# Optimization experiments

Measured on AMD Instinct MI355X. Metric: run time of the kernel, lower is better.

Reference implementation:

```python
import jax, jax.numpy as jnp
import numpy as np

N, D, B, K, H, E = 100000, 128, 4096, 64, 256, 128
DIN = D + 1
DELAYED_REWARD_STEP = 100.0


def setup_inputs() -> dict:
    key = jax.random.key(0)
    ks = jax.random.split(key, 16)
    s = 0.02
    d = {}
    d["node_pre_embedding"] = jax.random.normal(ks[0], (N, D), jnp.float32)
    d["steps"] = jax.random.uniform(ks[1], (B,), jnp.float32) * 50.0
    d["h0"] = jax.random.normal(ks[2], (B, H), jnp.float32) * 0.1
    d["c0"] = jax.random.normal(ks[3], (B, H), jnp.float32) * 0.1
    # MLP1: D_in -> 256 -> 128 (action embed, feeds LSTM input)
    d["W1a"] = jax.random.normal(ks[4], (256, DIN), jnp.float32) * s
    d["b1a"] = jnp.zeros((256,), jnp.float32)
    d["W1b"] = jax.random.normal(ks[5], (128, 256), jnp.float32) * s
    d["b1b"] = jnp.zeros((128,), jnp.float32)
    # MLP2: D_in -> 256 -> 128 (neighbor graph embed)
    d["W2a"] = jax.random.normal(ks[6], (256, DIN), jnp.float32) * s
    d["b2a"] = jnp.zeros((256,), jnp.float32)
    d["W2b"] = jax.random.normal(ks[7], (128, 256), jnp.float32) * s
    d["b2b"] = jnp.zeros((128,), jnp.float32)
    # MLP3: lstm_hidden (256) -> 128, single linear (hidden_dims3=[128])
    d["W3"] = jax.random.normal(ks[8], (E, H), jnp.float32) * s
    d["b3"] = jnp.zeros((E,), jnp.float32)
    # LSTMCell (PyTorch layout: gates i,f,g,o stacked on dim 0)
    d["Wih"] = jax.random.normal(ks[9], (4 * H, 128), jnp.float32) * s
    d["Whh"] = jax.random.normal(ks[10], (4 * H, H), jnp.float32) * s
    d["bih"] = jnp.zeros((4 * H,), jnp.float32)
    d["bhh"] = jnp.zeros((4 * H,), jnp.float32)
    # packed ragged adjacency: padded neighbor ids + per-row degree
    d["actions0"] = jax.random.randint(ks[11], (B,), 0, N)
    d["neighbors"] = jax.random.randint(ks[12], (B, K), 0, N)
    d["deg"] = jax.random.randint(ks[13], (B,), 1, K + 1)
    return d


def reference(node_pre_embedding, steps, h0, c0,
              W1a, b1a, W1b, b1b, W2a, b2a, W2b, b2b, W3, b3,
              Wih, Whh, bih, bhh, actions0, neighbors, deg):
    step_scaled = steps / DELAYED_REWARD_STEP  # [B]

    # --- graph embeddings for padded neighbors (ragged gather + MLP2) ---
    nei_feat = node_pre_embedding[neighbors]  # [B, K, D]
    step_col = jnp.broadcast_to(step_scaled[:, None, None], (B, K, 1))
    pre = jnp.concatenate([nei_feat, step_col], axis=-1)  # [B, K, D_in]
    g = jax.nn.relu(jnp.einsum('bkd,hd->bkh', pre, W2a) + b2a)
    g = jnp.einsum('bkh,eh->bke', g, W2b) + b2b  # [B, K, E]

    # --- action embedding: MLP1 -> LSTMCell -> MLP3 ---
    a_pre = jnp.concatenate([node_pre_embedding[actions0], step_scaled[:, None]], axis=-1)
    x = jax.nn.relu(a_pre @ W1a.T + b1a) @ W1b.T + b1b  # [B, 128]
    gates = x @ Wih.T + bih + h0 @ Whh.T + bhh  # [B, 4H]
    i, f, gg, o = jnp.split(gates, 4, axis=-1)
    c = jax.nn.sigmoid(f) * c0 + jax.nn.sigmoid(i) * jnp.tanh(gg)
    h = jax.nn.sigmoid(o) * jnp.tanh(c)
    emb = h @ W3.T + b3  # [B, E]

    # --- scaled dot-product scores, masked at padding ---
    vals = jnp.einsum('bke,be->bk', g, emb) / jnp.sqrt(jnp.float32(E))
    mask = jnp.arange(K)[None, :] < jnp.maximum(deg, 1)[:, None]
    vals = jnp.where(mask, vals, 0.0)
    return vals, h, c
```

## Files before the change

### kernel.cpp

```cpp
#include <hip/hip_runtime.h>
#include <hip/hip_bf16.h>

#define NN 100000
#define DD 128
#define BB 4096
#define KK 64
#define HH 256
#define EE 128

typedef __bf16 bf16x8 __attribute__((ext_vector_type(8)));
typedef float f32x4 __attribute__((ext_vector_type(4)));

#define EL_W1A 0
#define EL_W1B 32768
#define EL_WIH 65536
#define EL_WHH 196608
#define EL_W3  458752
#define EL_W2B 491520
#define EL_W2A 524288

#define BOFF_GB     0x110000
#define BOFF_W1COL  0x111000
#define BOFF_W2COL  0x111400
#define BOFF_CONST  0x111800
#define BOFF_X1     0x115800
#define BOFF_X      0x315800
#define BOFF_H0B    0x415800
#define BOFF_HB     0x615800
#define BOFF_EMB    0x815800
#define BOFF_T      0x915800

__device__ __forceinline__ float sigmoid_f(float x){ return 1.0f/(1.0f+__expf(-x)); }
__device__ __forceinline__ float tanh_f(float x){ return 1.0f - 2.0f/(__expf(2.0f*x)+1.0f); }

__device__ __forceinline__ bf16x8 pack8(float4 a, float4 b){
    bf16x8 v;
    v[0]=(__bf16)a.x; v[1]=(__bf16)a.y; v[2]=(__bf16)a.z; v[3]=(__bf16)a.w;
    v[4]=(__bf16)b.x; v[5]=(__bf16)b.y; v[6]=(__bf16)b.z; v[7]=(__bf16)b.w;
    return v;
}

__global__ __launch_bounds__(64) void swz_kernel(
    const float* __restrict__ W1a, const float* __restrict__ W1b,
    const float* __restrict__ Wih, const float* __restrict__ Whh,
    const float* __restrict__ W3,  const float* __restrict__ W2b,
    const float* __restrict__ W2a, const float* __restrict__ bih,
    const float* __restrict__ bhh, const float* __restrict__ h0,
    __bf16* __restrict__ wsbf, float* __restrict__ gb_ws,
    float* __restrict__ w1col_ws, float* __restrict__ w2col_ws,
    __bf16* __restrict__ h0_bf)
{
    int g = blockIdx.x, lane = threadIdx.x;
    if (g >= 1088){
        if (g < 1104){ int idx = (g-1088)*64 + lane; gb_ws[idx] = bih[idx] + bhh[idx]; }
        else if (g < 1108){ int idx = (g-1104)*64 + lane; w1col_ws[idx] = W1a[idx*129 + 128]; }
        else if (g < 1112){ int idx = (g-1108)*64 + lane; w2col_ws[idx] = W2a[idx*129 + 128]; }
        else {
            long i = (long)(g-1112)*64 + lane;
            const float4* sp = (const float4*)h0 + i*2;
            ((bf16x8*)h0_bf)[i] = pack8(sp[0], sp[1]);
        }
        return;
    }
    int quad = lane >> 4, l15 = lane & 15;
    const float* src; int stride, nkk, local; long dst; bool kn = false;
    if      (g <  64){ src=W1a; stride=129; nkk=4; dst=EL_W1A; local=g;      }
    else if (g < 128){ src=W1b; stride=256; nkk=8; dst=EL_W1B; local=g-64;   }
    else if (g < 384){ src=Wih; stride=128; nkk=4; dst=EL_WIH; local=g-128;  }
    else if (g < 896){ src=Whh; stride=256; nkk=8; dst=EL_WHH; local=g-384;  }
    else if (g < 960){ src=W3;  stride=256; nkk=8; dst=EL_W3;  local=g-896;  }
    else if (g <1024){ src=W2b; stride=256; nkk=4; dst=EL_W2B; local=g-960; kn=true; }
    else             { src=W2a; stride=129; nkk=4; dst=EL_W2A; local=g-1024; }
    int nt = local / nkk, kk = local % nkk;
    int n = nt*16 + l15, k0 = kk*32 + quad*8;
    bf16x8 v;
#pragma unroll
    for (int j = 0; j < 8; ++j){
        float x = kn ? src[(long)(k0+j)*stride + n] : src[(long)n*stride + k0 + j];
        v[j] = (__bf16)x;
    }
    ((bf16x8*)(wsbf + dst))[local*64 + lane] = v;
}

__global__ __launch_bounds__(64) void s1_kernel(
    const float* __restrict__ node_pre, const float* __restrict__ steps,
    const int* __restrict__ actions0, const float* __restrict__ b1a,
    const float* __restrict__ w1col, const __bf16* __restrict__ wsbf,
    __bf16* __restrict__ x1_bf)
{
    int lane = threadIdx.x, quad = lane >> 4, l15 = lane & 15;
    int mt = blockIdx.x >> 2, ng = blockIdx.x & 3, m0 = mt*16;
    long arow = actions0[m0 + l15];
    bf16x8 af[4];
#pragma unroll
    for (int kk = 0; kk < 4; ++kk){
        const float4* p = (const float4*)(node_pre + arow*128 + kk*32 + quad*8);
        af[kk] = pack8(p[0], p[1]);
    }
    float sb_i[4];
#pragma unroll
    for (int i = 0; i < 4; ++i) sb_i[i] = steps[m0 + quad*4 + i] * 0.01f;
    const bf16x8* FB = (const bf16x8*)(wsbf + EL_W1A);
#pragma unroll
    for (int j = 0; j < 4; ++j){
        int nt = ng*4 + j;
        f32x4 acc = {0.f,0.f,0.f,0.f};
#pragma unroll
        for (int kk = 0; kk < 4; ++kk)
            acc = __builtin_amdgcn_mfma_f32_16x16x32_bf16(af[kk], FB[(nt*4+kk)*64 + lane], acc, 0,0,0);
        int col = nt*16 + l15;
        float bb = b1a[col], wc = w1col[col];
#pragma unroll
        for (int i = 0; i < 4; ++i)
            x1_bf[(long)(m0 + quad*4 + i)*256 + col] = (__bf16)fmaxf(acc[i] + bb + wc*sb_i[i], 0.f);
    }
}

__global__ __launch_bounds__(64) void s2_kernel(
    const __bf16* __restrict__ x1_bf, const float* __restrict__ b1b,
    const __bf16* __restrict__ wsbf, __bf16* __restrict__ x_bf)
{
    int lane = threadIdx.x, quad = lane >> 4, l15 = lane & 15;
    int mt = blockIdx.x >> 2, ng = blockIdx.x & 3, m0 = mt*16;
    bf16x8 af[8];
#pragma unroll
    for (int kk = 0; kk < 8; ++kk)
        af[kk] = *(const bf16x8*)&x1_bf[(long)(m0 + l15)*256 + kk*32 + quad*8];
    const bf16x8* FB = (const bf16x8*)(wsbf + EL_W1B);
#pragma unroll
    for (int j = 0; j < 2; ++j){
        int nt = ng*2 + j;
        f32x4 acc = {0.f,0.f,0.f,0.f};
#pragma unroll
        for (int kk = 0; kk < 8; ++kk)
            acc = __builtin_amdgcn_mfma_f32_16x16x32_bf16(af[kk], FB[(nt*8+kk)*64 + lane], acc, 0,0,0);
        int col = nt*16 + l15;
        float bb = b1b[col];
#pragma unroll
        for (int i = 0; i < 4; ++i)
            x_bf[(long)(m0 + quad*4 + i)*128 + col] = (__bf16)(acc[i] + bb);
    }
}

__global__ __launch_bounds__(64) void lstm_kernel(
    const __bf16* __restrict__ x_bf, const __bf16* __restrict__ h0_bf,
    const float* __restrict__ c0_in, const float* __restrict__ gb_ws,
    const __bf16* __restrict__ wsbf,
    float* __restrict__ out_h, float* __restrict__ out_c, __bf16* __restrict__ h_bf)
{
    int lane = threadIdx.x, quad = lane >> 4, l15 = lane & 15;
    int mt = blockIdx.x >> 4, ct = blockIdx.x & 15, m0 = mt*16;
    bf16x8 af[12];
#pragma unroll
    for (int kk = 0; kk < 4; ++kk)
        af[kk] = *(const bf16x8*)&x_bf[(long)(m0 + l15)*128 + kk*32 + quad*8];
#pragma unroll
    for (int kk = 0; kk < 8; ++kk)
        af[4+kk] = *(const bf16x8*)&h0_bf[(long)(m0 + l15)*256 + kk*32 + quad*8];

    const bf16x8* FIH = (const bf16x8*)(wsbf + EL_WIH);
    const bf16x8* FHH = (const bf16x8*)(wsbf + EL_WHH);
    f32x4 aI = {0.f,0.f,0.f,0.f}, aF = aI, aG = aI, aO = aI;
#pragma unroll
    for (int kk = 0; kk < 4; ++kk){
        aI = __builtin_amdgcn_mfma_f32_16x16x32_bf16(af[kk], FIH[(( 0+ct)*4+kk)*64 + lane], aI, 0,0,0);
        aF = __builtin_amdgcn_mfma_f32_16x16x32_bf16(af[kk], FIH[((16+ct)*4+kk)*64 + lane], aF, 0,0,0);
        aG = __builtin_amdgcn_mfma_f32_16x16x32_bf16(af[kk], FIH[((32+ct)*4+kk)*64 + lane], aG, 0,0,0);
        aO = __builtin_amdgcn_mfma_f32_16x16x32_bf16(af[kk], FIH[((48+ct)*4+kk)*64 + lane], aO, 0,0,0);
    }
#pragma unroll
    for (int k2 = 0; k2 < 8; ++k2){
        aI = __builtin_amdgcn_mfma_f32_16x16x32_bf16(af[4+k2], FHH[(( 0+ct)*8+k2)*64 + lane], aI, 0,0,0);
        aF = __builtin_amdgcn_mfma_f32_16x16x32_bf16(af[4+k2], FHH[((16+ct)*8+k2)*64 + lane], aF, 0,0,0);
        aG = __builtin_amdgcn_mfma_f32_16x16x32_bf16(af[4+k2], FHH[((32+ct)*8+k2)*64 + lane], aG, 0,0,0);
        aO = __builtin_amdgcn_mfma_f32_16x16x32_bf16(af[4+k2], FHH[((48+ct)*8+k2)*64 + lane], aO, 0,0,0);
    }
    int col = ct*16 + l15;
    float bI = gb_ws[col], bF = gb_ws[256+col], bG = gb_ws[512+col], bO = gb_ws[768+col];
#pragma unroll
    for (int i = 0; i < 4; ++i){
        long row = m0 + quad*4 + i;
        float iv = aI[i]+bI, fv = aF[i]+bF, gv = aG[i]+bG, ov = aO[i]+bO;
        float cc = c0_in[row*256 + col];
        float cn = sigmoid_f(fv)*cc + sigmoid_f(iv)*tanh_f(gv);
        float hn = sigmoid_f(ov)*tanh_f(cn);
        out_c[row*256 + col] = cn;
        out_h[row*256 + col] = hn;
        h_bf[row*256 + col] = (__bf16)hn;
    }
}

__global__ __launch_bounds__(64) void s4_kernel(
    const __bf16* __restrict__ h_bf, const float* __restrict__ b3,
    const __bf16* __restrict__ wsbf, __bf16* __restrict__ emb_bf)
{
    int lane = threadIdx.x, quad = lane >> 4, l15 = lane & 15;
    int mt = blockIdx.x >> 2, ng = blockIdx.x & 3, m0 = mt*16;
    bf16x8 af[8];
#pragma unroll
    for (int kk = 0; kk < 8; ++kk)
        af[kk] = *(const bf16x8*)&h_bf[(long)(m0 + l15)*256 + kk*32 + quad*8];
    const bf16x8* FB = (const bf16x8*)(wsbf + EL_W3);
#pragma unroll
    for (int j = 0; j < 2; ++j){
        int nt = ng*2 + j;
        f32x4 acc = {0.f,0.f,0.f,0.f};
#pragma unroll
        for (int kk = 0; kk < 8; ++kk)
            acc = __builtin_amdgcn_mfma_f32_16x16x32_bf16(af[kk], FB[(nt*8+kk)*64 + lane], acc, 0,0,0);
        int col = nt*16 + l15;
        float bb = b3[col];
#pragma unroll
        for (int i = 0; i < 4; ++i)
            emb_bf[(long)(m0 + quad*4 + i)*128 + col] = (__bf16)(acc[i] + bb);
    }
}

__global__ __launch_bounds__(64) void s5_kernel(
    const __bf16* __restrict__ emb_bf, const float* __restrict__ b2b,
    const __bf16* __restrict__ wsbf, __bf16* __restrict__ t_bf,
    float* __restrict__ const_ws)
{
    int lane = threadIdx.x, quad = lane >> 4, l15 = lane & 15;
    int mt = blockIdx.x >> 2, ng = blockIdx.x & 3, m0 = mt*16;
    bf16x8 af[4];
#pragma unroll
    for (int kk = 0; kk < 4; ++kk)
        af[kk] = *(const bf16x8*)&emb_bf[(long)(m0 + l15)*128 + kk*32 + quad*8];
    if (ng == 0){
        float s = 0.f;
#pragma unroll
        for (int kk = 0; kk < 4; ++kk)
#pragma unroll
            for (int j = 0; j < 8; ++j)
                s += b2b[kk*32 + quad*8 + j] * (float)af[kk][j];
        s += __shfl_xor(s, 16, 64);
        s += __shfl_xor(s, 32, 64);
        if (lane < 16) const_ws[m0 + l15] = s;
    }
    const bf16x8* FB = (const bf16x8*)(wsbf + EL_W2B);
#pragma unroll
    for (int j = 0; j < 4; ++j){
        int nt = ng*4 + j;
        f32x4 acc = {0.f,0.f,0.f,0.f};
#pragma unroll
        for (int kk = 0; kk < 4; ++kk)
            acc = __builtin_amdgcn_mfma_f32_16x16x32_bf16(af[kk], FB[(nt*4+kk)*64 + lane], acc, 0,0,0);
        int col = nt*16 + l15;
#pragma unroll
        for (int i = 0; i < 4; ++i)
            t_bf[(long)(m0 + quad*4 + i)*256 + col] = (__bf16)acc[i];
    }
}

__global__ __launch_bounds__(256) void nei_kernel(
    const float* __restrict__ node_pre, const float* __restrict__ steps,
    const float* __restrict__ b2a, const float* __restrict__ w2col,
    const int* __restrict__ neighbors, const int* __restrict__ deg,
    const __bf16* __restrict__ wsbf, const __bf16* __restrict__ t_bf,
    const float* __restrict__ const_ws, float* __restrict__ out_vals)
{
    __shared__ __bf16 at[64*136];
    __shared__ float t_s[256], bias_s[256], vp[256];

    int tid = threadIdx.x, b = blockIdx.x;
    int degb = deg[b]; if (degb < 1) degb = 1;
    int ntile = (degb + 15) >> 4;
    float sb = steps[b] * 0.01f;
    t_s[tid]    = (float)t_bf[(long)b*256 + tid];
    bias_s[tid] = b2a[tid] + w2col[tid]*sb;
    {
        int r = tid >> 2, sg = tid & 3;
        if (r < ntile*16){
            long nb = neighbors[b*64 + r];
            const float4* sp = (const float4*)(node_pre + nb*128 + sg*32);
#pragma unroll
            for (int q = 0; q < 4; ++q){
                float4 fa = sp[q*2], fb = sp[q*2+1];
                *(bf16x8*)&at[r*136 + sg*32 + q*8] = pack8(fa, fb);
            }
        }
    }

    int wave = tid >> 6, lane = tid & 63, quad = lane >> 4, l15 = lane & 15;
    const bf16x8* FB = (const bf16x8*)(wsbf + EL_W2A);
    bf16x8 bw[16];
#pragma unroll
    for (int j = 0; j < 4; ++j){
        int nt = wave + 4*j;
#pragma unroll
        for (int kk = 0; kk < 4; ++kk) bw[j*4+kk] = FB[(nt*4+kk)*64 + lane];
    }
    __syncthreads();

#pragma unroll 1
    for (int mt = 0; mt < ntile; ++mt){
        bf16x8 af[4];
#pragma unroll
        for (int kk = 0; kk < 4; ++kk)
            af[kk] = *(const bf16x8*)&at[(mt*16 + l15)*136 + kk*32 + quad*8];
        f32x4 ps = {0.f,0.f,0.f,0.f};
#pragma unroll
        for (int j = 0; j < 4; ++j){
            int nt = wave + 4*j;
            f32x4 acc = {0.f,0.f,0.f,0.f};
#pragma unroll
            for (int kk = 0; kk < 4; ++kk)
                acc = __builtin_amdgcn_mfma_f32_16x16x32_bf16(af[kk], bw[j*4+kk], acc, 0,0,0);
            int col = nt*16 + l15;
            float bb = bias_s[col], tv = t_s[col];
#pragma unroll
            for (int i = 0; i < 4; ++i)
                ps[i] += fmaxf(acc[i] + bb, 0.f) * tv;
        }
#pragma unroll
        for (int m = 1; m < 16; m <<= 1){
#pragma unroll
            for (int i = 0; i < 4; ++i) ps[i] += __shfl_xor(ps[i], m, 64);
        }
        if (l15 == 0){
#pragma unroll
            for (int i = 0; i < 4; ++i) vp[wave*64 + mt*16 + quad*4 + i] = ps[i];
        }
    }
    __syncthreads();
    if (tid < 64){
        float v = vp[tid] + vp[64+tid] + vp[128+tid] + vp[192+tid];
        v = (v + const_ws[b]) * 0.08838834764831845f;
        if (tid >= degb) v = 0.f;
        out_vals[(long)b*64 + tid] = v;
    }
}

extern "C" void kernel_launch(void* const* d_in, const int* in_sizes, int n_in,
                              void* d_out, int out_size, void* d_ws, size_t ws_size,
                              hipStream_t stream)
{
    (void)in_sizes; (void)n_in; (void)out_size; (void)ws_size;
    const float* node_pre = (const float*)d_in[0];
    const float* steps    = (const float*)d_in[1];
    const float* h0       = (const float*)d_in[2];
    const float* c0       = (const float*)d_in[3];
    const float* W1a      = (const float*)d_in[4];
    const float* b1a      = (const float*)d_in[5];
    const float* W1b      = (const float*)d_in[6];
    const float* b1b      = (const float*)d_in[7];
    const float* W2a      = (const float*)d_in[8];
    const float* b2a      = (const float*)d_in[9];
    const float* W2b      = (const float*)d_in[10];
    const float* b2b      = (const float*)d_in[11];
    const float* W3       = (const float*)d_in[12];
    const float* b3       = (const float*)d_in[13];
    const float* Wih      = (const float*)d_in[14];
    const float* Whh      = (const float*)d_in[15];
    const float* bih      = (const float*)d_in[16];
    const float* bhh      = (const float*)d_in[17];
    const int* actions0   = (const int*)d_in[18];
    const int* neighbors  = (const int*)d_in[19];
    const int* deg        = (const int*)d_in[20];

    float* out      = (float*)d_out;
    float* out_vals = out;
    float* out_h    = out + (long)BB*KK;
    float* out_c    = out_h + (long)BB*HH;

    __bf16* wsbf     = (__bf16*)d_ws;
    float* gb_ws     = (float*)((char*)d_ws + BOFF_GB);
    float* w1col_ws  = (float*)((char*)d_ws + BOFF_W1COL);
    float* w2col_ws  = (float*)((char*)d_ws + BOFF_W2COL);
    float* const_ws  = (float*)((char*)d_ws + BOFF_CONST);
    __bf16* x1_bf    = (__bf16*)((char*)d_ws + BOFF_X1);
    __bf16* x_bf     = (__bf16*)((char*)d_ws + BOFF_X);
    __bf16* h0_bf    = (__bf16*)((char*)d_ws + BOFF_H0B);
    __bf16* h_bf     = (__bf16*)((char*)d_ws + BOFF_HB);
    __bf16* emb_bf   = (__bf16*)((char*)d_ws + BOFF_EMB);
    __bf16* t_bf     = (__bf16*)((char*)d_ws + BOFF_T);

    swz_kernel<<<dim3(3160), dim3(64), 0, stream>>>(W1a, W1b, Wih, Whh, W3, W2b, W2a,
                                                    bih, bhh, h0, wsbf, gb_ws,
                                                    w1col_ws, w2col_ws, h0_bf);
    s1_kernel<<<dim3(1024), dim3(64), 0, stream>>>(node_pre, steps, actions0, b1a,
                                                   w1col_ws, wsbf, x1_bf);
    s2_kernel<<<dim3(1024), dim3(64), 0, stream>>>(x1_bf, b1b, wsbf, x_bf);
    lstm_kernel<<<dim3(4096), dim3(64), 0, stream>>>(x_bf, h0_bf, c0, gb_ws, wsbf,
                                                     out_h, out_c, h_bf);
    s4_kernel<<<dim3(1024), dim3(64), 0, stream>>>(h_bf, b3, wsbf, emb_bf);
    s5_kernel<<<dim3(1024), dim3(64), 0, stream>>>(emb_bf, b2b, wsbf, t_bf, const_ws);
    nei_kernel<<<dim3(4096), dim3(256), 0, stream>>>(node_pre, steps, b2a, w2col_ws,
                                                     neighbors, deg, wsbf, t_bf, const_ws,
                                                     out_vals);
}
```

Before: 181.4 us.

## Fold linear layers algebraically and merge action-path stages into cooperative kernel

Precomputes Wih·W1b and W2b·W3 products plus their folded biases, which removes the separate s2 and s4/s5 GEMM stages. The remaining action-path stages (weight prep, s1, LSTM, t-projection) run in one cooperative persistent kernel with grid syncs, falling back to separate launches if the cooperative launch fails. h0 is now converted to bf16 inside the LSTM stage, removing a separate conversion pass. The folded-weight precompute uses slow scalar fp32 loops on every call, and grid-wide syncs add overhead in exchange for fewer launches.

```diff
diff --git a/kernel.cpp b/kernel.cpp
--- a/kernel.cpp
+++ b/kernel.cpp
@@ -1,4 +1,5 @@
 #include <hip/hip_runtime.h>
+#include <hip/hip_cooperative_groups.h>
 #include <hip/hip_bf16.h>
 
 #define NN 100000
@@ -11,24 +12,24 @@
 typedef __bf16 bf16x8 __attribute__((ext_vector_type(8)));
 typedef float f32x4 __attribute__((ext_vector_type(4)));
 
-#define EL_W1A 0
-#define EL_W1B 32768
-#define EL_WIH 65536
-#define EL_WHH 196608
-#define EL_W3  458752
-#define EL_W2B 491520
-#define EL_W2A 524288
-
-#define BOFF_GB     0x110000
-#define BOFF_W1COL  0x111000
-#define BOFF_W2COL  0x111400
-#define BOFF_CONST  0x111800
-#define BOFF_X1     0x115800
-#define BOFF_X      0x315800
-#define BOFF_H0B    0x415800
-#define BOFF_HB     0x615800
-#define BOFF_EMB    0x815800
-#define BOFF_T      0x915800
+#define EL_W1A   0
+#define EL_WHH   32768
+#define EL_W2A   294912
+#define EL_WFOLD 327680
+#define EL_TM    589824
+
+#define BOFF_GB2   0x140000
+#define BOFF_W1COL 0x141000
+#define BOFF_W2COL 0x141400
+#define BOFF_TB    0x141800
+#define BOFF_CVEC  0x141C00
+#define BOFF_CBIAS 0x142000
+#define BOFF_CONST 0x142400
+#define BOFF_X1    0x147000
+#define BOFF_HB    0x347000
+#define BOFF_T     0x547000
+
+#define N_PRE 1313
 
 __device__ __forceinline__ float sigmoid_f(float x){ return 1.0f/(1.0f+__expf(-x)); }
 __device__ __forceinline__ float tanh_f(float x){ return 1.0f - 2.0f/(__expf(2.0f*x)+1.0f); }
@@ -40,67 +41,108 @@
     return v;
 }
 
-__global__ __launch_bounds__(64) void swz_kernel(
-    const float* __restrict__ W1a, const float* __restrict__ W1b,
-    const float* __restrict__ Wih, const float* __restrict__ Whh,
-    const float* __restrict__ W3,  const float* __restrict__ W2b,
-    const float* __restrict__ W2a, const float* __restrict__ bih,
-    const float* __restrict__ bhh, const float* __restrict__ h0,
-    __bf16* __restrict__ wsbf, float* __restrict__ gb_ws,
-    float* __restrict__ w1col_ws, float* __restrict__ w2col_ws,
-    __bf16* __restrict__ h0_bf)
-{
-    int g = blockIdx.x, lane = threadIdx.x;
-    if (g >= 1088){
-        if (g < 1104){ int idx = (g-1088)*64 + lane; gb_ws[idx] = bih[idx] + bhh[idx]; }
-        else if (g < 1108){ int idx = (g-1104)*64 + lane; w1col_ws[idx] = W1a[idx*129 + 128]; }
-        else if (g < 1112){ int idx = (g-1108)*64 + lane; w2col_ws[idx] = W2a[idx*129 + 128]; }
-        else {
-            long i = (long)(g-1112)*64 + lane;
-            const float4* sp = (const float4*)h0 + i*2;
-            ((bf16x8*)h0_bf)[i] = pack8(sp[0], sp[1]);
-        }
-        return;
-    }
-    int quad = lane >> 4, l15 = lane & 15;
-    const float* src; int stride, nkk, local; long dst; bool kn = false;
-    if      (g <  64){ src=W1a; stride=129; nkk=4; dst=EL_W1A; local=g;      }
-    else if (g < 128){ src=W1b; stride=256; nkk=8; dst=EL_W1B; local=g-64;   }
-    else if (g < 384){ src=Wih; stride=128; nkk=4; dst=EL_WIH; local=g-128;  }
-    else if (g < 896){ src=Whh; stride=256; nkk=8; dst=EL_WHH; local=g-384;  }
-    else if (g < 960){ src=W3;  stride=256; nkk=8; dst=EL_W3;  local=g-896;  }
-    else if (g <1024){ src=W2b; stride=256; nkk=4; dst=EL_W2B; local=g-960; kn=true; }
-    else             { src=W2a; stride=129; nkk=4; dst=EL_W2A; local=g-1024; }
-    int nt = local / nkk, kk = local % nkk;
-    int n = nt*16 + l15, k0 = kk*32 + quad*8;
-    bf16x8 v;
-#pragma unroll
-    for (int j = 0; j < 8; ++j){
-        float x = kn ? src[(long)(k0+j)*stride + n] : src[(long)n*stride + k0 + j];
-        v[j] = (__bf16)x;
-    }
-    ((bf16x8*)(wsbf + dst))[local*64 + lane] = v;
-}
-
-__global__ __launch_bounds__(64) void s1_kernel(
-    const float* __restrict__ node_pre, const float* __restrict__ steps,
-    const int* __restrict__ actions0, const float* __restrict__ b1a,
-    const float* __restrict__ w1col, const __bf16* __restrict__ wsbf,
-    __bf16* __restrict__ x1_bf)
-{
-    int lane = threadIdx.x, quad = lane >> 4, l15 = lane & 15;
-    int mt = blockIdx.x >> 2, ng = blockIdx.x & 3, m0 = mt*16;
-    long arow = actions0[m0 + l15];
+struct ActP {
+    const float *node_pre, *steps, *h0, *c0;
+    const float *W1a, *b1a, *W1b, *b1b, *W2a, *W2b, *b2b, *W3, *b3;
+    const float *Wih, *Whh, *bih, *bhh;
+    const int   *actions0;
+    __bf16 *wsbf;
+    float  *gb2, *w1col, *w2col, *tb, *cvec, *cbias, *cst;
+    __bf16 *x1, *hb, *t;
+    float  *out_h, *out_c;
+};
+
+
+__device__ void stage_pre(const ActP& p, int g, int lane, int quad, int l15){
+    if (g < 640){
+        const float* src; int stride, nkk, local; long dst;
+        if      (g <  64){ src=p.W1a; stride=129; nkk=4; dst=EL_W1A; local=g;     }
+        else if (g < 576){ src=p.Whh; stride=256; nkk=8; dst=EL_WHH; local=g-64;  }
+        else             { src=p.W2a; stride=129; nkk=4; dst=EL_W2A; local=g-576; }
+        int nt = local / nkk, kk = local % nkk;
+        int n = nt*16 + l15, k0 = kk*32 + quad*8;
+        bf16x8 v;
+#pragma unroll
+        for (int j = 0; j < 8; ++j) v[j] = (__bf16)src[(long)n*stride + k0 + j];
+        ((bf16x8*)(p.wsbf + dst))[local*64 + lane] = v;
+    }
+    else if (g < 1152){
+        int c = (g-640)*64 + lane;
+        int grow = c >> 5, k8 = c & 31, k0 = k8*8;
+        float acc[8] = {0,0,0,0,0,0,0,0};
+        const float* wr = p.Wih + (long)grow*128;
+        for (int n = 0; n < 128; ++n){
+            float w = wr[n];
+            const float4* bp = (const float4*)(p.W1b + (long)n*256 + k0);
+            float4 b0 = bp[0], b1 = bp[1];
+            acc[0] += w*b0.x; acc[1] += w*b0.y; acc[2] += w*b0.z; acc[3] += w*b0.w;
+            acc[4] += w*b1.x; acc[5] += w*b1.y; acc[6] += w*b1.z; acc[7] += w*b1.w;
+        }
+        bf16x8 v;
+#pragma unroll
+        for (int j = 0; j < 8; ++j) v[j] = (__bf16)acc[j];
+        int nt = grow >> 4, l15r = grow & 15, kk = k8 >> 2, qd = k8 & 3;
+        ((bf16x8*)(p.wsbf + EL_WFOLD))[(nt*8+kk)*64 + qd*16 + l15r] = v;
+    }
+    else if (g < 1280){
+        int c = (g-1152)*64 + lane;
+        int hcol = c >> 5, m8 = c & 31, m0 = m8*8;
+        float acc[8] = {0,0,0,0,0,0,0,0};
+        for (int e = 0; e < 128; ++e){
+            float w = p.W2b[(long)e*256 + hcol];
+            const float4* wp = (const float4*)(p.W3 + (long)e*256 + m0);
+            float4 a0 = wp[0], a1 = wp[1];
+            acc[0] += w*a0.x; acc[1] += w*a0.y; acc[2] += w*a0.z; acc[3] += w*a0.w;
+            acc[4] += w*a1.x; acc[5] += w*a1.y; acc[6] += w*a1.z; acc[7] += w*a1.w;
+        }
+        bf16x8 v;
+#pragma unroll
+        for (int j = 0; j < 8; ++j) v[j] = (__bf16)acc[j];
+        int nt = hcol >> 4, l15r = hcol & 15, kk = m8 >> 2, qd = m8 & 3;
+        ((bf16x8*)(p.wsbf + EL_TM))[(nt*8+kk)*64 + qd*16 + l15r] = v;
+    }
+    else if (g < 1296){
+        int gi = (g-1280)*64 + lane;
+        float s = p.bih[gi] + p.bhh[gi];
+        const float* wr = p.Wih + (long)gi*128;
+        for (int n = 0; n < 128; ++n) s += wr[n]*p.b1b[n];
+        p.gb2[gi] = s;
+    }
+    else if (g < 1300){ int i = (g-1296)*64 + lane; p.w1col[i] = p.W1a[i*129 + 128]; }
+    else if (g < 1304){ int i = (g-1300)*64 + lane; p.w2col[i] = p.W2a[i*129 + 128]; }
+    else if (g < 1308){
+        int i = (g-1304)*64 + lane;
+        float s = 0.f;
+        for (int e = 0; e < 128; ++e) s += p.W2b[(long)e*256 + i]*p.b3[e];
+        p.tb[i] = s;
+    }
+    else if (g < 1312){
+        int i = (g-1308)*64 + lane;
+        float s = 0.f;
+        for (int e = 0; e < 128; ++e) s += p.b2b[e]*p.W3[(long)e*256 + i];
+        p.cvec[i] = s;
+    }
+    else {
+        float s = p.b2b[lane]*p.b3[lane] + p.b2b[lane+64]*p.b3[lane+64];
+#pragma unroll
+        for (int m = 1; m < 64; m <<= 1) s += __shfl_xor(s, m, 64);
+        if (lane == 0) p.cbias[0] = s;
+    }
+}
+
+__device__ void stage_s1(const ActP& p, int u, int lane, int quad, int l15){
+    int mt = u >> 2, ng = u & 3, m0 = mt*16;
+    long arow = p.actions0[m0 + l15];
     bf16x8 af[4];
 #pragma unroll
     for (int kk = 0; kk < 4; ++kk){
-        const float4* p = (const float4*)(node_pre + arow*128 + kk*32 + quad*8);
-        af[kk] = pack8(p[0], p[1]);
+        const float4* q = (const float4*)(p.node_pre + arow*128 + kk*32 + quad*8);
+        af[kk] = pack8(q[0], q[1]);
     }
     float sb_i[4];
 #pragma unroll
-    for (int i = 0; i < 4; ++i) sb_i[i] = steps[m0 + quad*4 + i] * 0.01f;
-    const bf16x8* FB = (const bf16x8*)(wsbf + EL_W1A);
+    for (int i = 0; i < 4; ++i) sb_i[i] = p.steps[m0 + quad*4 + i] * 0.01f;
+    const bf16x8* FB = (const bf16x8*)(p.wsbf + EL_W1A);
 #pragma unroll
     for (int j = 0; j < 4; ++j){
         int nt = ng*4 + j;
@@ -109,149 +151,110 @@
         for (int kk = 0; kk < 4; ++kk)
             acc = __builtin_amdgcn_mfma_f32_16x16x32_bf16(af[kk], FB[(nt*4+kk)*64 + lane], acc, 0,0,0);
         int col = nt*16 + l15;
-        float bb = b1a[col], wc = w1col[col];
+        float bb = p.b1a[col], wc = p.w1col[col];
 #pragma unroll
         for (int i = 0; i < 4; ++i)
-            x1_bf[(long)(m0 + quad*4 + i)*256 + col] = (__bf16)fmaxf(acc[i] + bb + wc*sb_i[i], 0.f);
-    }
-}
-
-__global__ __launch_bounds__(64) void s2_kernel(
-    const __bf16* __restrict__ x1_bf, const float* __restrict__ b1b,
-    const __bf16* __restrict__ wsbf, __bf16* __restrict__ x_bf)
-{
-    int lane = threadIdx.x, quad = lane >> 4, l15 = lane & 15;
-    int mt = blockIdx.x >> 2, ng = blockIdx.x & 3, m0 = mt*16;
+            p.x1[(long)(m0 + quad*4 + i)*256 + col] = (__bf16)fmaxf(acc[i] + bb + wc*sb_i[i], 0.f);
+    }
+}
+
+__device__ void stage_lstm(const ActP& p, int u, int lane, int quad, int l15){
+    int mt = u >> 4, ct = u & 15, m0 = mt*16;
+    bf16x8 af[16];
+#pragma unroll
+    for (int kk = 0; kk < 8; ++kk)
+        af[kk] = *(const bf16x8*)&p.x1[(long)(m0 + l15)*256 + kk*32 + quad*8];
+#pragma unroll
+    for (int kk = 0; kk < 8; ++kk){
+        const float4* hp = (const float4*)(p.h0 + (long)(m0 + l15)*256 + kk*32 + quad*8);
+        af[8+kk] = pack8(hp[0], hp[1]);
+    }
+    const bf16x8* FW = (const bf16x8*)(p.wsbf + EL_WFOLD);
+    const bf16x8* FH = (const bf16x8*)(p.wsbf + EL_WHH);
+    f32x4 aI = {0.f,0.f,0.f,0.f}, aF = aI, aG = aI, aO = aI;
+#pragma unroll 4
+    for (int kk = 0; kk < 8; ++kk){
+        aI = __builtin_amdgcn_mfma_f32_16x16x32_bf16(af[kk], FW[(( 0+ct)*8+kk)*64 + lane], aI, 0,0,0);
+        aF = __builtin_amdgcn_mfma_f32_16x16x32_bf16(af[kk], FW[((16+ct)*8+kk)*64 + lane], aF, 0,0,0);
+        aG = __builtin_amdgcn_mfma_f32_16x16x32_bf16(af[kk], FW[((32+ct)*8+kk)*64 + lane], aG, 0,0,0);
+        aO = __builtin_amdgcn_mfma_f32_16x16x32_bf16(af[kk], FW[((48+ct)*8+kk)*64 + lane], aO, 0,0,0);
+    }
+#pragma unroll 4
+    for (int kk = 0; kk < 8; ++kk){
+        aI = __builtin_amdgcn_mfma_f32_16x16x32_bf16(af[8+kk], FH[(( 0+ct)*8+kk)*64 + lane], aI, 0,0,0);
+        aF = __builtin_amdgcn_mfma_f32_16x16x32_bf16(af[8+kk], FH[((16+ct)*8+kk)*64 + lane], aF, 0,0,0);
+        aG = __builtin_amdgcn_mfma_f32_16x16x32_bf16(af[8+kk], FH[((32+ct)*8+kk)*64 + lane], aG, 0,0,0);
+        aO = __builtin_amdgcn_mfma_f32_16x16x32_bf16(af[8+kk], FH[((48+ct)*8+kk)*64 + lane], aO, 0,0,0);
+    }
+    int col = ct*16 + l15;
+    float bI = p.gb2[col], bF = p.gb2[256+col], bG = p.gb2[512+col], bO = p.gb2[768+col];
+#pragma unroll
+    for (int i = 0; i < 4; ++i){
+        long row = m0 + quad*4 + i;
+        float iv = aI[i]+bI, fv = aF[i]+bF, gv = aG[i]+bG, ov = aO[i]+bO;
+        float cc = p.c0[row*256 + col];
+        float cn = sigmoid_f(fv)*cc + sigmoid_f(iv)*tanh_f(gv);
+        float hn = sigmoid_f(ov)*tanh_f(cn);
+        p.out_c[row*256 + col] = cn;
+        p.out_h[row*256 + col] = hn;
+        p.hb[row*256 + col] = (__bf16)hn;
+    }
+}
+
+__device__ void stage_tk(const ActP& p, int u, int lane, int quad, int l15){
+    int mt = u >> 2, ng = u & 3, m0 = mt*16;
     bf16x8 af[8];
 #pragma unroll
     for (int kk = 0; kk < 8; ++kk)
-        af[kk] = *(const bf16x8*)&x1_bf[(long)(m0 + l15)*256 + kk*32 + quad*8];
-    const bf16x8* FB = (const bf16x8*)(wsbf + EL_W1B);
-#pragma unroll
-    for (int j = 0; j < 2; ++j){
-        int nt = ng*2 + j;
+        af[kk] = *(const bf16x8*)&p.hb[(long)(m0 + l15)*256 + kk*32 + quad*8];
+    if (ng == 0){
+        float s = 0.f;
+#pragma unroll
+        for (int kk = 0; kk < 8; ++kk)
+#pragma unroll
+            for (int j = 0; j < 8; ++j)
+                s += p.cvec[kk*32 + quad*8 + j] * (float)af[kk][j];
+        s += __shfl_xor(s, 16, 64);
+        s += __shfl_xor(s, 32, 64);
+        if (lane < 16) p.cst[m0 + l15] = s + p.cbias[0];
+    }
+    const bf16x8* FB = (const bf16x8*)(p.wsbf + EL_TM);
+#pragma unroll
+    for (int j = 0; j < 4; ++j){
+        int nt = ng*4 + j;
         f32x4 acc = {0.f,0.f,0.f,0.f};
 #pragma unroll
         for (int kk = 0; kk < 8; ++kk)
             acc = __builtin_amdgcn_mfma_f32_16x16x32_bf16(af[kk], FB[(nt*8+kk)*64 + lane], acc, 0,0,0);
         int col = nt*16 + l15;
-        float bb = b1b[col];
+        float bb = p.tb[col];
 #pragma unroll
         for (int i = 0; i < 4; ++i)
-            x_bf[(long)(m0 + quad*4 + i)*128 + col] = (__bf16)(acc[i] + bb);
-    }
-}
-
-__global__ __launch_bounds__(64) void lstm_kernel(
-    const __bf16* __restrict__ x_bf, const __bf16* __restrict__ h0_bf,
-    const float* __restrict__ c0_in, const float* __restrict__ gb_ws,
-    const __bf16* __restrict__ wsbf,
-    float* __restrict__ out_h, float* __restrict__ out_c, __bf16* __restrict__ h_bf)
+            p.t[(long)(m0 + quad*4 + i)*256 + col] = (__bf16)(acc[i] + bb);
+    }
+}
+
+__global__ __launch_bounds__(256, 2) void coop_act(ActP p)
 {
-    int lane = threadIdx.x, quad = lane >> 4, l15 = lane & 15;
-    int mt = blockIdx.x >> 4, ct = blockIdx.x & 15, m0 = mt*16;
-    bf16x8 af[12];
-#pragma unroll
-    for (int kk = 0; kk < 4; ++kk)
-        af[kk] = *(const bf16x8*)&x_bf[(long)(m0 + l15)*128 + kk*32 + quad*8];
-#pragma unroll
-    for (int kk = 0; kk < 8; ++kk)
-        af[4+kk] = *(const bf16x8*)&h0_bf[(long)(m0 + l15)*256 + kk*32 + quad*8];
-
-    const bf16x8* FIH = (const bf16x8*)(wsbf + EL_WIH);
-    const bf16x8* FHH = (const bf16x8*)(wsbf + EL_WHH);
-    f32x4 aI = {0.f,0.f,0.f,0.f}, aF = aI, aG = aI, aO = aI;
-#pragma unroll
-    for (int kk = 0; kk < 4; ++kk){
-        aI = __builtin_amdgcn_mfma_f32_16x16x32_bf16(af[kk], FIH[(( 0+ct)*4+kk)*64 + lane], aI, 0,0,0);
-        aF = __builtin_amdgcn_mfma_f32_16x16x32_bf16(af[kk], FIH[((16+ct)*4+kk)*64 + lane], aF, 0,0,0);
-        aG = __builtin_amdgcn_mfma_f32_16x16x32_bf16(af[kk], FIH[((32+ct)*4+kk)*64 + lane], aG, 0,0,0);
-        aO = __builtin_amdgcn_mfma_f32_16x16x32_bf16(af[kk], FIH[((48+ct)*4+kk)*64 + lane], aO, 0,0,0);
-    }
-#pragma unroll
-    for (int k2 = 0; k2 < 8; ++k2){
-        aI = __builtin_amdgcn_mfma_f32_16x16x32_bf16(af[4+k2], FHH[(( 0+ct)*8+k2)*64 + lane], aI, 0,0,0);
-        aF = __builtin_amdgcn_mfma_f32_16x16x32_bf16(af[4+k2], FHH[((16+ct)*8+k2)*64 + lane], aF, 0,0,0);
-        aG = __builtin_amdgcn_mfma_f32_16x16x32_bf16(af[4+k2], FHH[((32+ct)*8+k2)*64 + lane], aG, 0,0,0);
-        aO = __builtin_amdgcn_mfma_f32_16x16x32_bf16(af[4+k2], FHH[((48+ct)*8+k2)*64 + lane], aO, 0,0,0);
-    }
-    int col = ct*16 + l15;
-    float bI = gb_ws[col], bF = gb_ws[256+col], bG = gb_ws[512+col], bO = gb_ws[768+col];
-#pragma unroll
-    for (int i = 0; i < 4; ++i){
-        long row = m0 + quad*4 + i;
-        float iv = aI[i]+bI, fv = aF[i]+bF, gv = aG[i]+bG, ov = aO[i]+bO;
-        float cc = c0_in[row*256 + col];
-        float cn = sigmoid_f(fv)*cc + sigmoid_f(iv)*tanh_f(gv);
-        float hn = sigmoid_f(ov)*tanh_f(cn);
-        out_c[row*256 + col] = cn;
-        out_h[row*256 + col] = hn;
-        h_bf[row*256 + col] = (__bf16)hn;
-    }
-}
-
-__global__ __launch_bounds__(64) void s4_kernel(
-    const __bf16* __restrict__ h_bf, const float* __restrict__ b3,
-    const __bf16* __restrict__ wsbf, __bf16* __restrict__ emb_bf)
-{
-    int lane = threadIdx.x, quad = lane >> 4, l15 = lane & 15;
-    int mt = blockIdx.x >> 2, ng = blockIdx.x & 3, m0 = mt*16;
-    bf16x8 af[8];
-#pragma unroll
-    for (int kk = 0; kk < 8; ++kk)
-        af[kk] = *(const bf16x8*)&h_bf[(long)(m0 + l15)*256 + kk*32 + quad*8];
-    const bf16x8* FB = (const bf16x8*)(wsbf + EL_W3);
-#pragma unroll
-    for (int j = 0; j < 2; ++j){
-        int nt = ng*2 + j;
-        f32x4 acc = {0.f,0.f,0.f,0.f};
-#pragma unroll
-        for (int kk = 0; kk < 8; ++kk)
-            acc = __builtin_amdgcn_mfma_f32_16x16x32_bf16(af[kk], FB[(nt*8+kk)*64 + lane], acc, 0,0,0);
-        int col = nt*16 + l15;
-        float bb = b3[col];
-#pragma unroll
-        for (int i = 0; i < 4; ++i)
-            emb_bf[(long)(m0 + quad*4 + i)*128 + col] = (__bf16)(acc[i] + bb);
-    }
-}
-
-__global__ __launch_bounds__(64) void s5_kernel(
-    const __bf16* __restrict__ emb_bf, const float* __restrict__ b2b,
-    const __bf16* __restrict__ wsbf, __bf16* __restrict__ t_bf,
-    float* __restrict__ const_ws)
-{
-    int lane = threadIdx.x, quad = lane >> 4, l15 = lane & 15;
-    int mt = blockIdx.x >> 2, ng = blockIdx.x & 3, m0 = mt*16;
-    bf16x8 af[4];
-#pragma unroll
-    for (int kk = 0; kk < 4; ++kk)
-        af[kk] = *(const bf16x8*)&emb_bf[(long)(m0 + l15)*128 + kk*32 + quad*8];
-    if (ng == 0){
-        float s = 0.f;
-#pragma unroll
-        for (int kk = 0; kk < 4; ++kk)
-#pragma unroll
-            for (int j = 0; j < 8; ++j)
-                s += b2b[kk*32 + quad*8 + j] * (float)af[kk][j];
-        s += __shfl_xor(s, 16, 64);
-        s += __shfl_xor(s, 32, 64);
-        if (lane < 16) const_ws[m0 + l15] = s;
-    }
-    const bf16x8* FB = (const bf16x8*)(wsbf + EL_W2B);
-#pragma unroll
-    for (int j = 0; j < 4; ++j){
-        int nt = ng*4 + j;
-        f32x4 acc = {0.f,0.f,0.f,0.f};
-#pragma unroll
-        for (int kk = 0; kk < 4; ++kk)
-            acc = __builtin_amdgcn_mfma_f32_16x16x32_bf16(af[kk], FB[(nt*4+kk)*64 + lane], acc, 0,0,0);
-        int col = nt*16 + l15;
-#pragma unroll
-        for (int i = 0; i < 4; ++i)
-            t_bf[(long)(m0 + quad*4 + i)*256 + col] = (__bf16)acc[i];
-    }
-}
+    cooperative_groups::grid_group grid = cooperative_groups::this_grid();
+    const int tid = threadIdx.x, lane = tid & 63;
+    const int quad = lane >> 4, l15 = lane & 15;
+    const int gw = blockIdx.x*4 + (tid >> 6);
+    const int TW = gridDim.x*4;
+
+    for (int g = gw; g < N_PRE; g += TW) stage_pre(p, g, lane, quad, l15);
+    __threadfence(); grid.sync();
+    for (int u = gw; u < 1024; u += TW) stage_s1(p, u, lane, quad, l15);
+    __threadfence(); grid.sync();
+    for (int u = gw; u < 4096; u += TW) stage_lstm(p, u, lane, quad, l15);
+    __threadfence(); grid.sync();
+    for (int u = gw; u < 1024; u += TW) stage_tk(p, u, lane, quad, l15);
+}
+
+__global__ __launch_bounds__(64) void pre_k (ActP p){ int l = threadIdx.x; stage_pre (p, blockIdx.x, l, l>>4, l&15); }
+__global__ __launch_bounds__(64) void s1_k  (ActP p){ int l = threadIdx.x; stage_s1  (p, blockIdx.x, l, l>>4, l&15); }
+__global__ __launch_bounds__(64) void lstm_k(ActP p){ int l = threadIdx.x; stage_lstm(p, blockIdx.x, l, l>>4, l&15); }
+__global__ __launch_bounds__(64) void tk_k  (ActP p){ int l = threadIdx.x; stage_tk  (p, blockIdx.x, l, l>>4, l&15); }
 
 __global__ __launch_bounds__(256) void nei_kernel(
     const float* __restrict__ node_pre, const float* __restrict__ steps,
@@ -338,55 +341,58 @@
 {
     (void)in_sizes; (void)n_in; (void)out_size; (void)ws_size;
     const float* node_pre = (const float*)d_in[0];
-    const float* steps    = (const float*)d_in[1];
-    const float* h0       = (const float*)d_in[2];
-    const float* c0       = (const float*)d_in[3];
-    const float* W1a      = (const float*)d_in[4];
-    const float* b1a      = (const float*)d_in[5];
-    const float* W1b      = (const float*)d_in[6];
-    const float* b1b      = (const float*)d_in[7];
-    const float* W2a      = (const float*)d_in[8];
-    const float* b2a      = (const float*)d_in[9];
-    const float* W2b      = (const float*)d_in[10];
-    const float* b2b      = (const float*)d_in[11];
-    const float* W3       = (const float*)d_in[12];
-    const float* b3       = (const float*)d_in[13];
-    const float* Wih      = (const float*)d_in[14];
-    const float* Whh      = (const float*)d_in[15];
-    const float* bih      = (const float*)d_in[16];
-    const float* bhh      = (const float*)d_in[17];
-    const int* actions0   = (const int*)d_in[18];
-    const int* neighbors  = (const int*)d_in[19];
-    const int* deg        = (const int*)d_in[20];
 
     float* out      = (float*)d_out;
     float* out_vals = out;
     float* out_h    = out + (long)BB*KK;
     float* out_c    = out_h + (long)BB*HH;
 
-    __bf16* wsbf     = (__bf16*)d_ws;
-    float* gb_ws     = (float*)((char*)d_ws + BOFF_GB);
-    float* w1col_ws  = (float*)((char*)d_ws + BOFF_W1COL);
-    float* w2col_ws  = (float*)((char*)d_ws + BOFF_W2COL);
-    float* const_ws  = (float*)((char*)d_ws + BOFF_CONST);
-    __bf16* x1_bf    = (__bf16*)((char*)d_ws + BOFF_X1);
-    __bf16* x_bf     = (__bf16*)((char*)d_ws + BOFF_X);
-    __bf16* h0_bf    = (__bf16*)((char*)d_ws + BOFF_H0B);
-    __bf16* h_bf     = (__bf16*)((char*)d_ws + BOFF_HB);
-    __bf16* emb_bf   = (__bf16*)((char*)d_ws + BOFF_EMB);
-    __bf16* t_bf     = (__bf16*)((char*)d_ws + BOFF_T);
-
-    swz_kernel<<<dim3(3160), dim3(64), 0, stream>>>(W1a, W1b, Wih, Whh, W3, W2b, W2a,
-                                                    bih, bhh, h0, wsbf, gb_ws,
-                                                    w1col_ws, w2col_ws, h0_bf);
-    s1_kernel<<<dim3(1024), dim3(64), 0, stream>>>(node_pre, steps, actions0, b1a,
-                                                   w1col_ws, wsbf, x1_bf);
-    s2_kernel<<<dim3(1024), dim3(64), 0, stream>>>(x1_bf, b1b, wsbf, x_bf);
-    lstm_kernel<<<dim3(4096), dim3(64), 0, stream>>>(x_bf, h0_bf, c0, gb_ws, wsbf,
-                                                     out_h, out_c, h_bf);
-    s4_kernel<<<dim3(1024), dim3(64), 0, stream>>>(h_bf, b3, wsbf, emb_bf);
-    s5_kernel<<<dim3(1024), dim3(64), 0, stream>>>(emb_bf, b2b, wsbf, t_bf, const_ws);
-    nei_kernel<<<dim3(4096), dim3(256), 0, stream>>>(node_pre, steps, b2a, w2col_ws,
-                                                     neighbors, deg, wsbf, t_bf, const_ws,
-                                                     out_vals);
-}
+    ActP p;
+    p.node_pre = node_pre;
+    p.steps    = (const float*)d_in[1];
+    p.h0       = (const float*)d_in[2];
+    p.c0       = (const float*)d_in[3];
+    p.W1a      = (const float*)d_in[4];
+    p.b1a      = (const float*)d_in[5];
+    p.W1b      = (const float*)d_in[6];
+    p.b1b      = (const float*)d_in[7];
+    p.W2a      = (const float*)d_in[8];
+    p.W2b      = (const float*)d_in[10];
+    p.b2b      = (const float*)d_in[11];
+    p.W3       = (const float*)d_in[12];
+    p.b3       = (const float*)d_in[13];
+    p.Wih      = (const float*)d_in[14];
+    p.Whh      = (const float*)d_in[15];
+    p.bih      = (const float*)d_in[16];
+    p.bhh      = (const float*)d_in[17];
+    p.actions0 = (const int*)d_in[18];
+    p.wsbf  = (__bf16*)d_ws;
+    p.gb2   = (float*)((char*)d_ws + BOFF_GB2);
+    p.w1col = (float*)((char*)d_ws + BOFF_W1COL);
+    p.w2col = (float*)((char*)d_ws + BOFF_W2COL);
+    p.tb    = (float*)((char*)d_ws + BOFF_TB);
+    p.cvec  = (float*)((char*)d_ws + BOFF_CVEC);
+    p.cbias = (float*)((char*)d_ws + BOFF_CBIAS);
+    p.cst   = (float*)((char*)d_ws + BOFF_CONST);
+    p.x1    = (__bf16*)((char*)d_ws + BOFF_X1);
+    p.hb    = (__bf16*)((char*)d_ws + BOFF_HB);
+    p.t     = (__bf16*)((char*)d_ws + BOFF_T);
+    p.out_h = out_h; p.out_c = out_c;
+
+    void* kargs[] = { (void*)&p };
+    hipError_t ce = hipLaunchCooperativeKernel(coop_act, dim3(512), dim3(256),
+                                               kargs, 0, stream);
+    if (ce != hipSuccess){
+        pre_k <<<dim3(N_PRE), dim3(64), 0, stream>>>(p);
+        s1_k  <<<dim3(1024),  dim3(64), 0, stream>>>(p);
+        lstm_k<<<dim3(4096),  dim3(64), 0, stream>>>(p);
+        tk_k  <<<dim3(1024),  dim3(64), 0, stream>>>(p);
+    }
+
+    nei_kernel<<<dim3(4096), dim3(256), 0, stream>>>(
+        node_pre, p.steps, (const float*)d_in[9],
+        (const float*)((char*)d_ws + BOFF_W2COL),
+        (const int*)d_in[19], (const int*)d_in[20],
+        (const __bf16*)d_ws, (const __bf16*)((char*)d_ws + BOFF_T),
+        (const float*)((char*)d_ws + BOFF_CONST), out_vals);
+}
```

New measurement: 601.8 us. 3.32x slower.
